# Optimization experiments

Hardware: AMD Instinct MI355X
Metric: run time of the kernel (lower is better)

## Reference

```python
import jax, jax.numpy as jnp
import numpy as np

K, STRIDE, PAD = 3, 1, 1


def _unfold(x, k=K, stride=STRIDE, pad=PAD):
    # x: [B, C, H, W] -> patches [B, C*k*k, L] (im2col, torch nn.Unfold layout:
    # channel index = c*k*k + ki*k + kj)
    p = jax.lax.conv_general_dilated_patches(
        x, filter_shape=(k, k), window_strides=(stride, stride),
        padding=((pad, pad), (pad, pad)))  # [B, C*k*k, Ho, Wo]
    B = x.shape[0]
    return p.reshape(B, p.shape[1], -1)


def reference(x, weight, dweight, bias):
    B, C, H, W = x.shape
    O = weight.shape[0]
    cols = _unfold(x)                                   # [B, C*k*k, L]
    # scalar gate per spatial position: dweight . sigmoid(cols)
    gate = jnp.einsum('f,bfl->bl', dweight.reshape(-1), jax.nn.sigmoid(cols))
    gated = cols * gate[:, None, :]                     # [B, C*k*k, L]
    out = jnp.einsum('of,bfl->bol', weight.reshape(O, -1), gated)  # [B, O, L]
    out = out + bias[None, :, None]
    Ho, Wo = (H // 2, W // 2) if STRIDE == 2 else (H, W)
    return out.reshape(B, O, Ho, Wo)


def setup_inputs() -> dict:
    key = jax.random.key(0)
    k1, k2, k3, k4 = jax.random.split(key, 4)
    B, C, O, H, W = 8, 32, 32, 256, 256
    fan_out = O * K * K
    std = float(np.sqrt(2.0 / fan_out))
    return {
        'x': jax.random.normal(k1, (B, C, H, W), dtype=jnp.float32),
        'weight': jax.random.normal(k2, (O, C, K, K), dtype=jnp.float32) * std,
        'dweight': jax.random.normal(k3, (1, C, K, K), dtype=jnp.float32) * std,
        'bias': jax.random.normal(k4, (O,), dtype=jnp.float32),
    }
```

## Files before the change

kernel.cpp:

```cpp
#include <hip/hip_runtime.h>


typedef _Float16 half8 __attribute__((ext_vector_type(8)));
typedef float f32x16 __attribute__((ext_vector_type(16)));

#define BATCH 8
#define CIN 32
#define COUT 32
#define HH 256
#define WW 256
#define TW 32
#define TH 4
#define HTW 34
#define HTH 6
#define CSTR 40
#define NCHUNK 18
#define NLDSA 16
#define NPOS (HTH*HTW)

__global__ __launch_bounds__(256) void prep_pack(const float* __restrict__ w,
                                                 const float* __restrict__ dw,
                                                 _Float16* __restrict__ Apack,
                                                 float* __restrict__ dwf) {
  int t = blockIdx.x * 256 + threadIdx.x;
  if (t < 9216) {
    int q = t >> 9, lane = (t >> 3) & 63, j = t & 7;
    int tap = q >> 1, h = q & 1;
    int o = lane & 31, lh = lane >> 5;
    int c = h * 16 + lh * 8 + j;
    Apack[t] = (_Float16)w[o * 288 + c * 9 + tap];
  } else if (t < 9216 + 288) {
    int i = t - 9216;
    int tap = i >> 5, c = i & 31;
    dwf[i] = dw[c * 9 + tap];
  }
}

__global__ __launch_bounds__(256, 4) void dynconv(
    const float* __restrict__ x, const _Float16* __restrict__ Apack,
    const float* __restrict__ dwf, const float* __restrict__ bias,
    float* __restrict__ out) {
  __shared__ __align__(16) _Float16 lvA[NLDSA * 512];
  __shared__ __align__(16) _Float16 lv[NPOS * CSTR];
  __shared__ float gpart[9 * NPOS];

  const int bid0 = blockIdx.x;
  const int bb = bid0 & 7, idx = bid0 >> 3;
  const int xt = idx & 7, yt = idx >> 3;
  const int x0 = xt * TW, y0 = yt * TH;
  const int tid = threadIdx.x;
  const int lane = tid & 63;

  const half8 a16 = *(const half8*)(Apack + ((16 * 64 + lane) << 3));
  const half8 a17 = *(const half8*)(Apack + ((17 * 64 + lane) << 3));

  half8 acopy[4];
#pragma unroll
  for (int k = 0; k < 4; ++k)
    acopy[k] = *(const half8*)(Apack + ((k * 256 + tid) << 3));

  const bool owner = tid < NPOS;
  float v[CIN];
  if (owner) {
    const int yy = tid / HTW, xx = tid - (tid / HTW) * HTW;
    const int gy = y0 + yy - 1, gx = x0 + xx - 1;
    const int voff = (gy << 8) + gx;
    if ((unsigned)gy < 256u && (unsigned)gx < 256u) {
#pragma unroll
      for (int c = 0; c < CIN; ++c)
        v[c] = x[(((size_t)(bb * CIN + c)) << 16) + voff];
    } else {
#pragma unroll
      for (int c = 0; c < CIN; ++c) v[c] = 0.f;
    }
  }

#pragma unroll
  for (int k = 0; k < 4; ++k)
    *(half8*)(lvA + ((k * 256 + tid) << 3)) = acopy[k];

  if (owner) {
    float p[9];
#pragma unroll
    for (int tap = 0; tap < 9; ++tap) p[tap] = 0.f;
    _Float16 hv[CIN];
#pragma unroll
    for (int c = 0; c < CIN; ++c) {
      const float s = __builtin_amdgcn_rcpf(1.f + __expf(-v[c]));
#pragma unroll
      for (int tap = 0; tap < 9; ++tap)
        p[tap] += dwf[tap * 32 + c] * s;
      hv[c] = (_Float16)v[c];
    }
#pragma unroll
    for (int u = 0; u < 4; ++u)
      *(half8*)(lv + tid * CSTR + u * 8) = *(const half8*)(hv + u * 8);
#pragma unroll
    for (int tap = 0; tap < 9; ++tap)
      gpart[tap * NPOS + tid] = p[tap];
  }
  __syncthreads();

  const int w8 = tid >> 6;
  const int ln = lane & 31, lh = lane >> 5;

  float gate = 0.f;
#pragma unroll
  for (int ki = 0; ki < 3; ++ki)
#pragma unroll
    for (int kj = 0; kj < 3; ++kj)
      gate += gpart[(ki * 3 + kj) * NPOS + (w8 + ki) * HTW + ln + kj];

  f32x16 acc;
#pragma unroll
  for (int i = 0; i < 16; ++i) acc[i] = 0.f;

#pragma unroll
  for (int q = 0; q < NCHUNK; ++q) {
    const int tap = q >> 1, h = q & 1;
    const int ki = tap / 3, kj = tap - ki * 3;
    const half8 a = (q < NLDSA)
                        ? *(const half8*)(lvA + ((q * 64 + lane) << 3))
                        : (q == 16 ? a16 : a17);
    const int off = ((w8 + ki) * HTW + ln + kj) * CSTR + h * 16 + lh * 8;
    const half8 bv = *(const half8*)(lv + off);
    acc = __builtin_amdgcn_mfma_f32_32x32x16_f16(a, bv, acc, 0, 0, 0);
  }

  const int voff_out = ((y0 + w8) << 8) + x0 + ln;
#pragma unroll
  for (int reg = 0; reg < 16; ++reg) {
    const int o = (reg & 3) + 8 * (reg >> 2) + 4 * lh;
    out[(((size_t)(bb * COUT + o)) << 16) + voff_out] = acc[reg] * gate + bias[o];
  }
}

extern "C" void kernel_launch(void* const* d_in, const int* in_sizes, int n_in,
                              void* d_out, int out_size, void* d_ws, size_t ws_size,
                              hipStream_t stream) {
  const float* x    = (const float*)d_in[0];
  const float* wgt  = (const float*)d_in[1];
  const float* dw   = (const float*)d_in[2];
  const float* bias = (const float*)d_in[3];
  float* out = (float*)d_out;

  _Float16* Apack = (_Float16*)d_ws;
  float* dwf      = (float*)((char*)d_ws + 18432);

  prep_pack<<<(9216 + 288 + 255) / 256, 256, 0, stream>>>(wgt, dw, Apack, dwf);
  dynconv<<<BATCH * (HH / TH) * (WW / TW), 256, 0, stream>>>(x, Apack, dwf, bias, out);
}
```

Measured before the change: 138.5 us.

## Cut LDS footprint and use packed fp16 dot for gate to raise occupancy

Result: no change. 138.2 us (-0.2%).

```diff
diff --git a/kernel.cpp b/kernel.cpp
--- a/kernel.cpp
+++ b/kernel.cpp
@@ -2,6 +2,7 @@
 
 
 typedef _Float16 half8 __attribute__((ext_vector_type(8)));
+typedef _Float16 half2 __attribute__((ext_vector_type(2)));
 typedef float f32x16 __attribute__((ext_vector_type(16)));
 
 #define BATCH 8
@@ -15,13 +16,14 @@
 #define HTH 6
 #define CSTR 40
 #define NCHUNK 18
-#define NLDSA 16
+#define NLDSA 12
+#define NREGA (NCHUNK - NLDSA)
 #define NPOS (HTH*HTW)
 
 __global__ __launch_bounds__(256) void prep_pack(const float* __restrict__ w,
                                                  const float* __restrict__ dw,
                                                  _Float16* __restrict__ Apack,
-                                                 float* __restrict__ dwf) {
+                                                 half2* __restrict__ dwf2) {
   int t = blockIdx.x * 256 + threadIdx.x;
   if (t < 9216) {
     int q = t >> 9, lane = (t >> 3) & 63, j = t & 7;
@@ -29,20 +31,23 @@
     int o = lane & 31, lh = lane >> 5;
     int c = h * 16 + lh * 8 + j;
     Apack[t] = (_Float16)w[o * 288 + c * 9 + tap];
-  } else if (t < 9216 + 288) {
+  } else if (t < 9216 + 144) {
     int i = t - 9216;
-    int tap = i >> 5, c = i & 31;
-    dwf[i] = dw[c * 9 + tap];
+    int cp = i / 9, tap = i - cp * 9;
+    half2 d;
+    d.x = (_Float16)dw[(2 * cp) * 9 + tap];
+    d.y = (_Float16)dw[(2 * cp + 1) * 9 + tap];
+    dwf2[i] = d;
   }
 }
 
-__global__ __launch_bounds__(256, 4) void dynconv(
+__global__ __launch_bounds__(256, 5) void dynconv(
     const float* __restrict__ x, const _Float16* __restrict__ Apack,
-    const float* __restrict__ dwf, const float* __restrict__ bias,
+    const half2* __restrict__ dwf2, const float* __restrict__ bias,
     float* __restrict__ out) {
   __shared__ __align__(16) _Float16 lvA[NLDSA * 512];
   __shared__ __align__(16) _Float16 lv[NPOS * CSTR];
-  __shared__ float gpart[9 * NPOS];
+  __shared__ _Float16 gpart[9 * NPOS];
 
   const int bid0 = blockIdx.x;
   const int bb = bid0 & 7, idx = bid0 >> 3;
@@ -51,12 +56,14 @@
   const int tid = threadIdx.x;
   const int lane = tid & 63;
 
-  const half8 a16 = *(const half8*)(Apack + ((16 * 64 + lane) << 3));
-  const half8 a17 = *(const half8*)(Apack + ((17 * 64 + lane) << 3));
+  half8 areg[NREGA];
+#pragma unroll
+  for (int r = 0; r < NREGA; ++r)
+    areg[r] = *(const half8*)(Apack + (((NLDSA + r) * 64 + lane) << 3));
 
-  half8 acopy[4];
+  half8 acopy[3];
 #pragma unroll
-  for (int k = 0; k < 4; ++k)
+  for (int k = 0; k < 3; ++k)
     acopy[k] = *(const half8*)(Apack + ((k * 256 + tid) << 3));
 
   const bool owner = tid < NPOS;
@@ -76,7 +83,7 @@
   }
 
 #pragma unroll
-  for (int k = 0; k < 4; ++k)
+  for (int k = 0; k < 3; ++k)
     *(half8*)(lvA + ((k * 256 + tid) << 3)) = acopy[k];
 
   if (owner) {
@@ -85,19 +92,31 @@
     for (int tap = 0; tap < 9; ++tap) p[tap] = 0.f;
     _Float16 hv[CIN];
 #pragma unroll
-    for (int c = 0; c < CIN; ++c) {
-      const float s = __builtin_amdgcn_rcpf(1.f + __expf(-v[c]));
+    for (int cp = 0; cp < CIN / 2; ++cp) {
+      const float v0 = v[2 * cp], v1 = v[2 * cp + 1];
+      const float s0 = __builtin_amdgcn_rcpf(1.f + __expf(-v0));
+      const float s1 = __builtin_amdgcn_rcpf(1.f + __expf(-v1));
+      half2 s2;
+      s2.x = (_Float16)s0;
+      s2.y = (_Float16)s1;
+      hv[2 * cp] = (_Float16)v0;
+      hv[2 * cp + 1] = (_Float16)v1;
 #pragma unroll
-      for (int tap = 0; tap < 9; ++tap)
-        p[tap] += dwf[tap * 32 + c] * s;
-      hv[c] = (_Float16)v[c];
+      for (int tap = 0; tap < 9; ++tap) {
+        const half2 d2 = dwf2[cp * 9 + tap];
+#if __has_builtin(__builtin_amdgcn_fdot2)
+        p[tap] = __builtin_amdgcn_fdot2(s2, d2, p[tap], false);
+#else
+        p[tap] += (float)s2.x * (float)d2.x + (float)s2.y * (float)d2.y;
+#endif
+      }
     }
 #pragma unroll
     for (int u = 0; u < 4; ++u)
       *(half8*)(lv + tid * CSTR + u * 8) = *(const half8*)(hv + u * 8);
 #pragma unroll
     for (int tap = 0; tap < 9; ++tap)
-      gpart[tap * NPOS + tid] = p[tap];
+      gpart[tap * NPOS + tid] = (_Float16)p[tap];
   }
   __syncthreads();
 
@@ -109,7 +128,7 @@
   for (int ki = 0; ki < 3; ++ki)
 #pragma unroll
     for (int kj = 0; kj < 3; ++kj)
-      gate += gpart[(ki * 3 + kj) * NPOS + (w8 + ki) * HTW + ln + kj];
+      gate += (float)gpart[(ki * 3 + kj) * NPOS + (w8 + ki) * HTW + ln + kj];
 
   f32x16 acc;
 #pragma unroll
@@ -121,7 +140,7 @@
     const int ki = tap / 3, kj = tap - ki * 3;
     const half8 a = (q < NLDSA)
                         ? *(const half8*)(lvA + ((q * 64 + lane) << 3))
-                        : (q == 16 ? a16 : a17);
+                        : areg[q - NLDSA];
     const int off = ((w8 + ki) * HTW + ln + kj) * CSTR + h * 16 + lh * 8;
     const half8 bv = *(const half8*)(lv + off);
     acc = __builtin_amdgcn_mfma_f32_32x32x16_f16(a, bv, acc, 0, 0, 0);
@@ -145,8 +164,8 @@
   float* out = (float*)d_out;
 
   _Float16* Apack = (_Float16*)d_ws;
-  float* dwf      = (float*)((char*)d_ws + 18432);
+  half2* dwf2     = (half2*)((char*)d_ws + 18432);
 
-  prep_pack<<<(9216 + 288 + 255) / 256, 256, 0, stream>>>(wgt, dw, Apack, dwf);
-  dynconv<<<BATCH * (HH / TH) * (WW / TW), 256, 0, stream>>>(x, Apack, dwf, bias, out);
+  prep_pack<<<(9216 + 144 + 255) / 256, 256, 0, stream>>>(wgt, dw, Apack, dwf2);
+  dynconv<<<BATCH * (HH / TH) * (WW / TW), 256, 0, stream>>>(x, Apack, dwf2, bias, out);
 }
```
